# Optimization experiments

Measured on AMD Instinct MI355X. Metric: run time of the kernel, lower is better.

The kernel has to match this reference:

```python
import jax, jax.numpy as jnp
import numpy as np

INPUT_SIZE = 63
HIDDEN = 128
NUM_CLASSES = 11
B, T = 4096, 128


def _gru_layer(x_seq, w_ih, w_hh, b_ih, b_hh):
    """PyTorch-semantics GRU layer. x_seq: [B,T,D] -> outputs [B,T,H]."""
    Bsz = x_seq.shape[0]
    H = w_hh.shape[1]
    # Precompute input projections for all timesteps in one big GEMM: [B,T,3H]
    gates_x = jnp.einsum('btd,gd->btg', x_seq, w_ih) + b_ih

    def step(h, gx):
        gh = h @ w_hh.T + b_hh                       # [B,3H]
        xr, xz, xn = jnp.split(gx, 3, axis=-1)
        hr, hz, hn = jnp.split(gh, 3, axis=-1)
        r = jax.nn.sigmoid(xr + hr)
        z = jax.nn.sigmoid(xz + hz)
        n = jnp.tanh(xn + r * hn)
        h_new = (1.0 - z) * n + z * h
        return h_new, h_new

    h0 = jnp.zeros((Bsz, H), x_seq.dtype)
    _, ys = jax.lax.scan(step, h0, jnp.swapaxes(gates_x, 0, 1))  # ys: [T,B,H]
    return jnp.swapaxes(ys, 0, 1)


def setup_inputs() -> dict:
    key = jax.random.key(0)
    ks = jax.random.split(key, 13)
    s_ih0 = 1.0 / np.sqrt(HIDDEN)
    u = lambda k, shape, s: jax.random.uniform(k, shape, jnp.float32, -s, s)
    inp = {
        'x': jax.random.normal(ks[0], (B, T, INPUT_SIZE), jnp.float32),
        # GRU layer 0: input_size=63 -> hidden=128
        'w_ih0': u(ks[1], (3 * HIDDEN, INPUT_SIZE), s_ih0),
        'w_hh0': u(ks[2], (3 * HIDDEN, HIDDEN), s_ih0),
        'b_ih0': u(ks[3], (3 * HIDDEN,), s_ih0),
        'b_hh0': u(ks[4], (3 * HIDDEN,), s_ih0),
        # GRU layer 1: hidden -> hidden
        'w_ih1': u(ks[5], (3 * HIDDEN, HIDDEN), s_ih0),
        'w_hh1': u(ks[6], (3 * HIDDEN, HIDDEN), s_ih0),
        'b_ih1': u(ks[7], (3 * HIDDEN,), s_ih0),
        'b_hh1': u(ks[8], (3 * HIDDEN,), s_ih0),
        # classifier: Linear(128,64) -> ReLU -> Linear(64,11)
        'w1': u(ks[9], (64, HIDDEN), 1.0 / np.sqrt(HIDDEN)),
        'b1': u(ks[10], (64,), 1.0 / np.sqrt(HIDDEN)),
        'w2': u(ks[11], (NUM_CLASSES, 64), 1.0 / np.sqrt(64)),
        'b2': u(ks[12], (NUM_CLASSES,), 1.0 / np.sqrt(64)),
    }
    return inp


def reference(x, w_ih0, w_hh0, b_ih0, b_hh0, w_ih1, w_hh1, b_ih1, b_hh1, w1, b1, w2, b2):
    h1 = _gru_layer(x, w_ih0, w_hh0, b_ih0, b_hh0)    # [B,T,H]
    h2 = _gru_layer(h1, w_ih1, w_hh1, b_ih1, b_hh1)   # [B,T,H]
    last = h2[:, -1, :]                               # [B,H]
    hidden = jax.nn.relu(last @ w1.T + b1)            # [B,64] (dropout is identity in eval)
    return hidden @ w2.T + b2                         # [B,num_classes]
```

## Files before the change

### kernel.cpp

```cpp
#include <hip/hip_runtime.h>
#include <hip/hip_bf16.h>

typedef __attribute__((ext_vector_type(8))) short s8v;
typedef __attribute__((ext_vector_type(4))) float f4v;

#define MF(A, B, C) C = __builtin_amdgcn_mfma_f32_16x16x32_bf16((A), (B), (C), 0, 0, 0)

__device__ __forceinline__ ushort f2bf(float f) {
  unsigned u = __float_as_uint(f);
  u += 0x7FFF + ((u >> 16) & 1);
  return (ushort)(u >> 16);
}
__device__ __forceinline__ float bf2f(ushort h) {
  return __uint_as_float(((unsigned)h) << 16);
}
__device__ __forceinline__ float sigm(float p) { return 1.f / (1.f + __expf(-p)); }
__device__ __forceinline__ float tanh_safe(float a) {
  float t = __expf(-2.f * fabsf(a));
  float ng = (1.f - t) / (1.f + t);
  return a < 0.f ? -ng : ng;
}
__device__ __forceinline__ float dot4(float4 a, float4 b) {
  return fmaf(a.x, b.x, fmaf(a.y, b.y, fmaf(a.z, b.z, a.w * b.w)));
}

__global__ void conv_x(const float* __restrict__ x, ushort* __restrict__ xhi,
                       ushort* __restrict__ xlo, int total) {
  int idx = blockIdx.x * 256 + threadIdx.x;
  if (idx >= total) return;
  int k4 = (idx & 15) * 4;
  long bt = idx >> 4;
  #pragma unroll
  for (int j = 0; j < 4; ++j) {
    int k = k4 + j;
    float v = (k < 63) ? x[bt * 63 + k] : 0.f;
    ushort hi = f2bf(v);
    xhi[bt * 64 + k] = hi;
    xlo[bt * 64 + k] = f2bf(v - bf2f(hi));
  }
}

__global__ void pack_fr(const float* __restrict__ src, ushort* __restrict__ dst,
                        int Kreal, int KT, int total) {
  int idx = blockIdx.x * 256 + threadIdx.x;
  if (idx >= total) return;
  int i = idx & 7, l = (idx >> 3) & 63, hl = (idx >> 9) & 1;
  int rest = idx >> 10;
  int kt = rest % KT, nt = rest / KT;
  int g = nt * 16 + (l & 15);
  int k = kt * 32 + (l >> 4) * 8 + i;
  float v = (k < Kreal) ? src[g * Kreal + k] : 0.f;
  ushort hi = f2bf(v);
  dst[idx] = hl ? f2bf(v - bf2f(hi)) : hi;
}

__global__ void __attribute__((amdgpu_flat_work_group_size(512, 512),
                               amdgpu_waves_per_eu(2, 2)))
rec_l0(const ushort* __restrict__ xhi, const ushort* __restrict__ xlo,
       const ushort* __restrict__ fih, const ushort* __restrict__ fhh,
       const float* __restrict__ bi, const float* __restrict__ bh,
       ushort* __restrict__ s_hi, ushort* __restrict__ s_lo,
       ushort* __restrict__ c_hi, ushort* __restrict__ c_lo,
       int t0, int tc, int first)
{
  __shared__ __align__(16) ushort hh_[2][2048], hl_[2][2048];
  __shared__ __align__(16) float bb[512];
  const int tid = threadIdx.x;
  const int l = tid & 63, wv = tid >> 6;
  const int lr = l & 15, lg = l >> 4;
  const long b0 = (long)blockIdx.x * 16;

  if (tid < 128) {
    bb[tid]       = bi[tid] + bh[tid];
    bb[128 + tid] = bi[128 + tid] + bh[128 + tid];
    bb[256 + tid] = bi[256 + tid];
    bb[384 + tid] = bh[256 + tid];
  }
  const int u0 = (wv << 4) + (lg << 2);
  const int hb = lr * 256 + ((u0 << 1) ^ ((lr & 7) << 4));
  if (first) {
    *(ushort4*)((char*)hh_[0] + hb) = make_ushort4(0, 0, 0, 0);
    *(ushort4*)((char*)hl_[0] + hb) = make_ushort4(0, 0, 0, 0);
  } else {
    *(ushort4*)((char*)hh_[0] + hb) = *(const ushort4*)&c_hi[(b0 + lr) * 128 + u0];
    *(ushort4*)((char*)hl_[0] + hb) = *(const ushort4*)&c_lo[(b0 + lr) * 128 + u0];
  }

  s8v Ba[12];
  s8v Bb[24];
  #pragma unroll
  for (int gi = 0; gi < 3; ++gi) {
    int nt = wv + 8 * gi;
    #pragma unroll
    for (int kt = 0; kt < 2; ++kt)
      #pragma unroll
      for (int hl = 0; hl < 2; ++hl)
        Ba[(gi * 2 + kt) * 2 + hl] = *(const s8v*)&fih[((long)((nt * 2 + kt) * 2 + hl)) * 512 + l * 8];
    #pragma unroll
    for (int kt = 0; kt < 4; ++kt)
      #pragma unroll
      for (int hl = 0; hl < 2; ++hl)
        Bb[(gi * 4 + kt) * 2 + hl] = *(const s8v*)&fhh[((long)((nt * 4 + kt) * 2 + hl)) * 512 + l * 8];
  }

  s8v xch[2], xcl[2], xnh[2], xnl[2];
  {
    long xo = ((b0 + lr) * 128 + t0) * 64 + lg * 8;
    xch[0] = *(const s8v*)&xhi[xo]; xch[1] = *(const s8v*)&xhi[xo + 32];
    xcl[0] = *(const s8v*)&xlo[xo]; xcl[1] = *(const s8v*)&xlo[xo + 32];
  }
  __syncthreads();

  int pp = 0;
  for (int s = 0; s < tc; ++s, pp ^= 1) {
    if (s + 1 < tc) {
      long xo = ((b0 + lr) * 128 + (t0 + s + 1)) * 64 + lg * 8;
      xnh[0] = *(const s8v*)&xhi[xo]; xnh[1] = *(const s8v*)&xhi[xo + 32];
      xnl[0] = *(const s8v*)&xlo[xo]; xnl[1] = *(const s8v*)&xlo[xo + 32];
    }
    f4v ar = {0.f, 0.f, 0.f, 0.f}, az = ar, anx = ar, anh = ar;
    #pragma unroll
    for (int kt = 0; kt < 4; ++kt) {
      int ba = lr * 256 + ((kt * 64 + lg * 16) ^ ((lr & 7) << 4));
      s8v Ah = *(const s8v*)((const char*)hh_[pp] + ba);
      s8v Al = *(const s8v*)((const char*)hl_[pp] + ba);
      MF(Bb[(0 * 4 + kt) * 2 + 0], Ah, ar);
      MF(Bb[(1 * 4 + kt) * 2 + 0], Ah, az);
      MF(Bb[(2 * 4 + kt) * 2 + 0], Ah, anh);
      MF(Bb[(0 * 4 + kt) * 2 + 1], Ah, ar);
      MF(Bb[(1 * 4 + kt) * 2 + 1], Ah, az);
      MF(Bb[(2 * 4 + kt) * 2 + 1], Ah, anh);
      MF(Bb[(0 * 4 + kt) * 2 + 0], Al, ar);
      MF(Bb[(1 * 4 + kt) * 2 + 0], Al, az);
      MF(Bb[(2 * 4 + kt) * 2 + 0], Al, anh);
    }
    #pragma unroll
    for (int kt = 0; kt < 2; ++kt) {
      MF(Ba[(0 * 2 + kt) * 2 + 0], xch[kt], ar);
      MF(Ba[(1 * 2 + kt) * 2 + 0], xch[kt], az);
      MF(Ba[(2 * 2 + kt) * 2 + 0], xch[kt], anx);
      MF(Ba[(0 * 2 + kt) * 2 + 1], xch[kt], ar);
      MF(Ba[(1 * 2 + kt) * 2 + 1], xch[kt], az);
      MF(Ba[(2 * 2 + kt) * 2 + 1], xch[kt], anx);
      MF(Ba[(0 * 2 + kt) * 2 + 0], xcl[kt], ar);
      MF(Ba[(1 * 2 + kt) * 2 + 0], xcl[kt], az);
      MF(Ba[(2 * 2 + kt) * 2 + 0], xcl[kt], anx);
    }
    {
      ushort4 oh = *(const ushort4*)((const char*)hh_[pp] + hb);
      ushort4 ol = *(const ushort4*)((const char*)hl_[pp] + hb);
      f4v vbr = *(const f4v*)&bb[u0];
      f4v vbz = *(const f4v*)&bb[128 + u0];
      f4v vbx = *(const f4v*)&bb[256 + u0];
      f4v vbh = *(const f4v*)&bb[384 + u0];
      const ushort* ohp = (const ushort*)&oh;
      const ushort* olp = (const ushort*)&ol;
      ushort nh_[4], nl_[4];
      #pragma unroll
      for (int j = 0; j < 4; ++j) {
        float hold = bf2f(ohp[j]) + bf2f(olp[j]);
        float rg = sigm(ar[j] + vbr[j]);
        float zg = sigm(az[j] + vbz[j]);
        float ng = tanh_safe(anx[j] + vbx[j] + rg * (anh[j] + vbh[j]));
        float hn = (1.f - zg) * ng + zg * hold;
        ushort hbf = f2bf(hn);
        nh_[j] = hbf; nl_[j] = f2bf(hn - bf2f(hbf));
      }
      ushort4 wh = make_ushort4(nh_[0], nh_[1], nh_[2], nh_[3]);
      ushort4 wl = make_ushort4(nl_[0], nl_[1], nl_[2], nl_[3]);
      *(ushort4*)((char*)hh_[pp ^ 1] + hb) = wh;
      *(ushort4*)((char*)hl_[pp ^ 1] + hb) = wl;
      long so = ((long)s * 4096 + b0 + lr) * 128 + u0;
      *(ushort4*)&s_hi[so] = wh;
      *(ushort4*)&s_lo[so] = wl;
    }
    xch[0] = xnh[0]; xch[1] = xnh[1]; xcl[0] = xnl[0]; xcl[1] = xnl[1];
    __syncthreads();
  }
  *(ushort4*)&c_hi[(b0 + lr) * 128 + u0] = *(const ushort4*)((const char*)hh_[pp] + hb);
  *(ushort4*)&c_lo[(b0 + lr) * 128 + u0] = *(const ushort4*)((const char*)hl_[pp] + hb);
}

__global__ void __attribute__((amdgpu_flat_work_group_size(512, 512),
                               amdgpu_waves_per_eu(2, 2)))
rec_l1(const ushort* __restrict__ s_hi, const ushort* __restrict__ s_lo,
       const ushort* __restrict__ fih, const ushort* __restrict__ fhh,
       const float* __restrict__ bi, const float* __restrict__ bh,
       ushort* __restrict__ c_hi, ushort* __restrict__ c_lo,
       float* __restrict__ h1f, int tc, int first, int last)
{
  __shared__ __align__(16) ushort hh_[2][2048], hl_[2][2048];
  __shared__ __align__(16) ushort gh_[2][2048], gl_[2][2048];
  __shared__ __align__(16) float bb[512];
  const int tid = threadIdx.x;
  const int l = tid & 63, wv = tid >> 6;
  const int lr = l & 15, lg = l >> 4;
  const long b0 = (long)blockIdx.x * 16;

  if (tid < 128) {
    bb[tid]       = bi[tid] + bh[tid];
    bb[128 + tid] = bi[128 + tid] + bh[128 + tid];
    bb[256 + tid] = bi[256 + tid];
    bb[384 + tid] = bh[256 + tid];
  }
  const int u0 = (wv << 4) + (lg << 2);
  const int hb = lr * 256 + ((u0 << 1) ^ ((lr & 7) << 4));
  if (first) {
    *(ushort4*)((char*)hh_[0] + hb) = make_ushort4(0, 0, 0, 0);
    *(ushort4*)((char*)hl_[0] + hb) = make_ushort4(0, 0, 0, 0);
  } else {
    *(ushort4*)((char*)hh_[0] + hb) = *(const ushort4*)&c_hi[(b0 + lr) * 128 + u0];
    *(ushort4*)((char*)hl_[0] + hb) = *(const ushort4*)&c_lo[(b0 + lr) * 128 + u0];
  }

  const int stid = tid & 255;
  const int srow = stid >> 4, sc16 = stid & 15;
  const int sdst = srow * 256 + ((sc16 * 16) ^ ((srow & 7) << 4));
  const ushort* ssel = (tid < 256) ? s_hi : s_lo;
  ushort* dsel = (tid < 256) ? &gh_[0][0] : &gl_[0][0];

  s8v Ba[24], Bb[24];
  #pragma unroll
  for (int gi = 0; gi < 3; ++gi) {
    int nt = wv + 8 * gi;
    #pragma unroll
    for (int kt = 0; kt < 4; ++kt)
      #pragma unroll
      for (int hl = 0; hl < 2; ++hl) {
        Ba[(gi * 4 + kt) * 2 + hl] = *(const s8v*)&fih[((long)((nt * 4 + kt) * 2 + hl)) * 512 + l * 8];
        Bb[(gi * 4 + kt) * 2 + hl] = *(const s8v*)&fhh[((long)((nt * 4 + kt) * 2 + hl)) * 512 + l * 8];
      }
  }
  {
    s8v v = *(const s8v*)&ssel[((long)0 * 4096 + b0 + srow) * 128 + sc16 * 8];
    *(s8v*)((char*)(dsel + 0 * 2048) + sdst) = v;
  }
  __syncthreads();

  int pp = 0;
  for (int tl = 0; tl < tc; ++tl, pp ^= 1) {
    s8v sreg;
    const int havenext = (tl + 1 < tc);
    if (havenext)
      sreg = *(const s8v*)&ssel[((long)(tl + 1) * 4096 + b0 + srow) * 128 + sc16 * 8];

    f4v ar = {0.f, 0.f, 0.f, 0.f}, az = ar, anx = ar, anh = ar;
    #pragma unroll
    for (int kt = 0; kt < 4; ++kt) {
      int ba = lr * 256 + ((kt * 64 + lg * 16) ^ ((lr & 7) << 4));
      s8v Hh = *(const s8v*)((const char*)hh_[pp] + ba);
      s8v Hl = *(const s8v*)((const char*)hl_[pp] + ba);
      s8v Gh = *(const s8v*)((const char*)gh_[pp] + ba);
      s8v Gl = *(const s8v*)((const char*)gl_[pp] + ba);
      MF(Bb[(0 * 4 + kt) * 2 + 0], Hh, ar);
      MF(Ba[(0 * 4 + kt) * 2 + 0], Gh, ar);
      MF(Bb[(1 * 4 + kt) * 2 + 0], Hh, az);
      MF(Ba[(1 * 4 + kt) * 2 + 0], Gh, az);
      MF(Bb[(2 * 4 + kt) * 2 + 0], Hh, anh);
      MF(Ba[(2 * 4 + kt) * 2 + 0], Gh, anx);
      MF(Bb[(0 * 4 + kt) * 2 + 1], Hh, ar);
      MF(Ba[(0 * 4 + kt) * 2 + 1], Gh, ar);
      MF(Bb[(1 * 4 + kt) * 2 + 1], Hh, az);
      MF(Ba[(1 * 4 + kt) * 2 + 1], Gh, az);
      MF(Bb[(2 * 4 + kt) * 2 + 1], Hh, anh);
      MF(Ba[(2 * 4 + kt) * 2 + 1], Gh, anx);
      MF(Bb[(0 * 4 + kt) * 2 + 0], Hl, ar);
      MF(Ba[(0 * 4 + kt) * 2 + 0], Gl, ar);
      MF(Bb[(1 * 4 + kt) * 2 + 0], Hl, az);
      MF(Ba[(1 * 4 + kt) * 2 + 0], Gl, az);
      MF(Bb[(2 * 4 + kt) * 2 + 0], Hl, anh);
      MF(Ba[(2 * 4 + kt) * 2 + 0], Gl, anx);
    }
    {
      ushort4 oh = *(const ushort4*)((const char*)hh_[pp] + hb);
      ushort4 ol = *(const ushort4*)((const char*)hl_[pp] + hb);
      f4v vbr = *(const f4v*)&bb[u0];
      f4v vbz = *(const f4v*)&bb[128 + u0];
      f4v vbx = *(const f4v*)&bb[256 + u0];
      f4v vbh = *(const f4v*)&bb[384 + u0];
      const ushort* ohp = (const ushort*)&oh;
      const ushort* olp = (const ushort*)&ol;
      ushort nh_[4], nl_[4];
      #pragma unroll
      for (int j = 0; j < 4; ++j) {
        float hold = bf2f(ohp[j]) + bf2f(olp[j]);
        float rg = sigm(ar[j] + vbr[j]);
        float zg = sigm(az[j] + vbz[j]);
        float ng = tanh_safe(anx[j] + vbx[j] + rg * (anh[j] + vbh[j]));
        float hn = (1.f - zg) * ng + zg * hold;
        ushort hbf = f2bf(hn);
        nh_[j] = hbf; nl_[j] = f2bf(hn - bf2f(hbf));
      }
      *(ushort4*)((char*)hh_[pp ^ 1] + hb) = make_ushort4(nh_[0], nh_[1], nh_[2], nh_[3]);
      *(ushort4*)((char*)hl_[pp ^ 1] + hb) = make_ushort4(nl_[0], nl_[1], nl_[2], nl_[3]);
    }
    if (havenext)
      *(s8v*)((char*)(dsel + (size_t)(pp ^ 1) * 2048) + sdst) = sreg;
    __syncthreads();
  }
  {
    ushort4 fh = *(const ushort4*)((const char*)hh_[pp] + hb);
    ushort4 fl = *(const ushort4*)((const char*)hl_[pp] + hb);
    *(ushort4*)&c_hi[(b0 + lr) * 128 + u0] = fh;
    *(ushort4*)&c_lo[(b0 + lr) * 128 + u0] = fl;
    if (last) {
      const ushort* fhp = (const ushort*)&fh;
      const ushort* flp = (const ushort*)&fl;
      float4 o;
      o.x = bf2f(fhp[0]) + bf2f(flp[0]);
      o.y = bf2f(fhp[1]) + bf2f(flp[1]);
      o.z = bf2f(fhp[2]) + bf2f(flp[2]);
      o.w = bf2f(fhp[3]) + bf2f(flp[3]);
      *(float4*)&h1f[(b0 + lr) * 128 + u0] = o;
    }
  }
}

__global__ __launch_bounds__(512) void head_k(
    const float* __restrict__ h1f, const float* __restrict__ w1,
    const float* __restrict__ b1, const float* __restrict__ w2,
    const float* __restrict__ b2, float* __restrict__ out)
{
  __shared__ float hrow[16][132];
  __shared__ float w1s[64][132];
  __shared__ float hid[16][68];
  const int tid = threadIdx.x;
  const long b0 = (long)blockIdx.x * 16;
  for (int i = tid; i < 64 * 128; i += 512) w1s[i >> 7][i & 127] = w1[i];
  {
    int rr = tid >> 5, k4 = (tid & 31) * 4;
    *(float4*)&hrow[rr][k4] = *(const float4*)&h1f[(b0 + rr) * 128 + k4];
  }
  __syncthreads();
  {
    int r = tid & 15, fu = tid >> 4;
    float a0 = 0.f, a1 = 0.f;
    for (int k4 = 0; k4 < 32; ++k4) {
      float4 hv = *(const float4*)&hrow[r][k4 * 4];
      float4 wa = *(const float4*)&w1s[fu][k4 * 4];
      float4 wb = *(const float4*)&w1s[fu + 32][k4 * 4];
      a0 += dot4(wa, hv);
      a1 += dot4(wb, hv);
    }
    a0 += b1[fu]; a1 += b1[fu + 32];
    hid[r][fu]      = fmaxf(a0, 0.f);
    hid[r][fu + 32] = fmaxf(a1, 0.f);
  }
  __syncthreads();
  if (tid < 176) {
    int rr = tid / 11, c = tid - rr * 11;
    float acc = b2[c];
    for (int k = 0; k < 64; ++k) acc = fmaf(w2[c * 64 + k], hid[rr][k], acc);
    out[(b0 + rr) * 11 + c] = acc;
  }
}

extern "C" void kernel_launch(void* const* d_in, const int* in_sizes, int n_in,
                              void* d_out, int out_size, void* d_ws, size_t ws_size,
                              hipStream_t stream) {
  (void)in_sizes; (void)n_in; (void)out_size;
  const float* x    = (const float*)d_in[0];
  const float* wih0 = (const float*)d_in[1];
  const float* whh0 = (const float*)d_in[2];
  const float* bih0 = (const float*)d_in[3];
  const float* bhh0 = (const float*)d_in[4];
  const float* wih1 = (const float*)d_in[5];
  const float* whh1 = (const float*)d_in[6];
  const float* bih1 = (const float*)d_in[7];
  const float* bhh1 = (const float*)d_in[8];
  const float* w1   = (const float*)d_in[9];
  const float* b1   = (const float*)d_in[10];
  const float* w2   = (const float*)d_in[11];
  const float* b2   = (const float*)d_in[12];

  char* wsb = (char*)d_ws;
  size_t o = 0;
  ushort* fih0 = (ushort*)(wsb + o); o += 98304;
  ushort* fhh0 = (ushort*)(wsb + o); o += 196608;
  ushort* fih1 = (ushort*)(wsb + o); o += 196608;
  ushort* fhh1 = (ushort*)(wsb + o); o += 196608;
  ushort* xhi  = (ushort*)(wsb + o); o += 67108864ULL;
  ushort* xlo  = (ushort*)(wsb + o); o += 67108864ULL;
  ushort* hc0h = (ushort*)(wsb + o); o += 1048576;
  ushort* hc0l = (ushort*)(wsb + o); o += 1048576;
  ushort* hc1h = (ushort*)(wsb + o); o += 1048576;
  ushort* hc1l = (ushort*)(wsb + o); o += 1048576;
  float*  h1f  = (float*)(wsb + o);  o += 2097152;

  long rem = (long)ws_size - (long)o;
  long tcmax = rem / (2 * 1048576L);
  int Tc = tcmax > 128 ? 128 : (int)tcmax;
  if (Tc < 1) return;
  ushort* sh = (ushort*)(wsb + o);
  ushort* sl = sh + (long)Tc * 524288;

  hipLaunchKernelGGL(conv_x, dim3(32768), dim3(256), 0, stream, x, xhi, xlo, 8388608);
  hipLaunchKernelGGL(pack_fr, dim3(192), dim3(256), 0, stream, wih0, fih0, 63, 2, 49152);
  hipLaunchKernelGGL(pack_fr, dim3(384), dim3(256), 0, stream, whh0, fhh0, 128, 4, 98304);
  hipLaunchKernelGGL(pack_fr, dim3(384), dim3(256), 0, stream, wih1, fih1, 128, 4, 98304);
  hipLaunchKernelGGL(pack_fr, dim3(384), dim3(256), 0, stream, whh1, fhh1, 128, 4, 98304);

  for (int t0 = 0; t0 < 128; t0 += Tc) {
    int tc = (128 - t0) < Tc ? (128 - t0) : Tc;
    hipLaunchKernelGGL(rec_l0, dim3(256), dim3(512), 0, stream,
                       xhi, xlo, fih0, fhh0, bih0, bhh0, sh, sl, hc0h, hc0l,
                       t0, tc, (int)(t0 == 0));
    hipLaunchKernelGGL(rec_l1, dim3(256), dim3(512), 0, stream,
                       sh, sl, fih1, fhh1, bih1, bhh1, hc1h, hc1l, h1f,
                       tc, (int)(t0 == 0), (int)(t0 + tc == 128));
  }
  hipLaunchKernelGGL(head_k, dim3(256), dim3(512), 0, stream,
                     h1f, w1, b1, w2, b2, (float*)d_out);
}
```

Before: 676.0 us.

## Split layer-0 GRU recurrence MFMAs across two wave groups with LDS reduction

Doubles the rec_l0 block to 1024 threads. Eight waves compute the hi-weight products and the hi·lo cross term, while eight more compute the lo-weight products and write partial sums to shared memory. The hi waves then add those partials and apply the gate math. The extra waves also stage the next timestep of x into shared memory, replacing per-lane global loads. This halves weight registers and MFMA chain length per wave, which should shorten the serial per-step latency. The cost is an extra block barrier per step plus an LDS round trip for the partials.

```diff
diff --git a/kernel.cpp b/kernel.cpp
--- a/kernel.cpp
+++ b/kernel.cpp
@@ -54,8 +54,8 @@
   dst[idx] = hl ? f2bf(v - bf2f(hi)) : hi;
 }
 
-__global__ void __attribute__((amdgpu_flat_work_group_size(512, 512),
-                               amdgpu_waves_per_eu(2, 2)))
+__global__ void __attribute__((amdgpu_flat_work_group_size(1024, 1024),
+                               amdgpu_waves_per_eu(4, 4)))
 rec_l0(const ushort* __restrict__ xhi, const ushort* __restrict__ xlo,
        const ushort* __restrict__ fih, const ushort* __restrict__ fhh,
        const float* __restrict__ bi, const float* __restrict__ bh,
@@ -65,9 +65,15 @@
 {
   __shared__ __align__(16) ushort hh_[2][2048], hl_[2][2048];
   __shared__ __align__(16) float bb[512];
+  __shared__ __align__(16) ushort xs[2][2][16][76];
+  __shared__ __align__(16) float pd[8][4][256];
+
   const int tid = threadIdx.x;
-  const int l = tid & 63, wv = tid >> 6;
+  const int wv = tid >> 6, l = tid & 63;
   const int lr = l & 15, lg = l >> 4;
+  const int isHi = (wv < 8);
+  const int p = wv & 7;
+  const int lsw = l ^ (l >> 3);
   const long b0 = (long)blockIdx.x * 16;
 
   if (tid < 128) {
@@ -76,77 +82,103 @@
     bb[256 + tid] = bi[256 + tid];
     bb[384 + tid] = bh[256 + tid];
   }
-  const int u0 = (wv << 4) + (lg << 2);
+  const int u0 = (p << 4) + (lg << 2);
   const int hb = lr * 256 + ((u0 << 1) ^ ((lr & 7) << 4));
-  if (first) {
-    *(ushort4*)((char*)hh_[0] + hb) = make_ushort4(0, 0, 0, 0);
-    *(ushort4*)((char*)hl_[0] + hb) = make_ushort4(0, 0, 0, 0);
-  } else {
-    *(ushort4*)((char*)hh_[0] + hb) = *(const ushort4*)&c_hi[(b0 + lr) * 128 + u0];
-    *(ushort4*)((char*)hl_[0] + hb) = *(const ushort4*)&c_lo[(b0 + lr) * 128 + u0];
-  }
-
-  s8v Ba[12];
-  s8v Bb[24];
+  if (isHi) {
+    if (first) {
+      *(ushort4*)((char*)hh_[0] + hb) = make_ushort4(0, 0, 0, 0);
+      *(ushort4*)((char*)hl_[0] + hb) = make_ushort4(0, 0, 0, 0);
+    } else {
+      *(ushort4*)((char*)hh_[0] + hb) = *(const ushort4*)&c_hi[(b0 + lr) * 128 + u0];
+      *(ushort4*)((char*)hl_[0] + hb) = *(const ushort4*)&c_lo[(b0 + lr) * 128 + u0];
+    }
+  }
+
+  const int hls = isHi ? 0 : 1;
+  s8v Fih[6];
+  s8v Fhh[12];
   #pragma unroll
   for (int gi = 0; gi < 3; ++gi) {
-    int nt = wv + 8 * gi;
+    int nt = p + 8 * gi;
     #pragma unroll
     for (int kt = 0; kt < 2; ++kt)
-      #pragma unroll
-      for (int hl = 0; hl < 2; ++hl)
-        Ba[(gi * 2 + kt) * 2 + hl] = *(const s8v*)&fih[((long)((nt * 2 + kt) * 2 + hl)) * 512 + l * 8];
+      Fih[gi * 2 + kt] = *(const s8v*)&fih[((long)((nt * 2 + kt) * 2 + hls)) * 512 + l * 8];
     #pragma unroll
     for (int kt = 0; kt < 4; ++kt)
-      #pragma unroll
-      for (int hl = 0; hl < 2; ++hl)
-        Bb[(gi * 4 + kt) * 2 + hl] = *(const s8v*)&fhh[((long)((nt * 4 + kt) * 2 + hl)) * 512 + l * 8];
-  }
-
-  s8v xch[2], xcl[2], xnh[2], xnl[2];
-  {
-    long xo = ((b0 + lr) * 128 + t0) * 64 + lg * 8;
-    xch[0] = *(const s8v*)&xhi[xo]; xch[1] = *(const s8v*)&xhi[xo + 32];
-    xcl[0] = *(const s8v*)&xlo[xo]; xcl[1] = *(const s8v*)&xlo[xo + 32];
+      Fhh[gi * 4 + kt] = *(const s8v*)&fhh[((long)((nt * 4 + kt) * 2 + hls)) * 512 + l * 8];
+  }
+
+  const int sid = (wv - 8) * 64 + l;
+  const int spl = sid >> 8, sq = sid & 255;
+  const int srow = sq >> 4, sc8 = sq & 15;
+  const ushort* xsrc = spl ? xlo : xhi;
+
+  if (!isHi) {
+    ushort4 v = *(const ushort4*)&xsrc[((b0 + srow) * 128 + t0) * 64 + sc8 * 4];
+    *(ushort4*)&xs[0][spl][srow][sc8 * 4] = v;
   }
   __syncthreads();
 
   int pp = 0;
   for (int s = 0; s < tc; ++s, pp ^= 1) {
-    if (s + 1 < tc) {
-      long xo = ((b0 + lr) * 128 + (t0 + s + 1)) * 64 + lg * 8;
-      xnh[0] = *(const s8v*)&xhi[xo]; xnh[1] = *(const s8v*)&xhi[xo + 32];
-      xnl[0] = *(const s8v*)&xlo[xo]; xnl[1] = *(const s8v*)&xlo[xo + 32];
-    }
+    const int havenext = (s + 1 < tc);
+    ushort4 xr;
+    if (!isHi && havenext)
+      xr = *(const ushort4*)&xsrc[((b0 + srow) * 128 + (t0 + s + 1)) * 64 + sc8 * 4];
+
     f4v ar = {0.f, 0.f, 0.f, 0.f}, az = ar, anx = ar, anh = ar;
-    #pragma unroll
-    for (int kt = 0; kt < 4; ++kt) {
-      int ba = lr * 256 + ((kt * 64 + lg * 16) ^ ((lr & 7) << 4));
-      s8v Ah = *(const s8v*)((const char*)hh_[pp] + ba);
-      s8v Al = *(const s8v*)((const char*)hl_[pp] + ba);
-      MF(Bb[(0 * 4 + kt) * 2 + 0], Ah, ar);
-      MF(Bb[(1 * 4 + kt) * 2 + 0], Ah, az);
-      MF(Bb[(2 * 4 + kt) * 2 + 0], Ah, anh);
-      MF(Bb[(0 * 4 + kt) * 2 + 1], Ah, ar);
-      MF(Bb[(1 * 4 + kt) * 2 + 1], Ah, az);
-      MF(Bb[(2 * 4 + kt) * 2 + 1], Ah, anh);
-      MF(Bb[(0 * 4 + kt) * 2 + 0], Al, ar);
-      MF(Bb[(1 * 4 + kt) * 2 + 0], Al, az);
-      MF(Bb[(2 * 4 + kt) * 2 + 0], Al, anh);
-    }
-    #pragma unroll
-    for (int kt = 0; kt < 2; ++kt) {
-      MF(Ba[(0 * 2 + kt) * 2 + 0], xch[kt], ar);
-      MF(Ba[(1 * 2 + kt) * 2 + 0], xch[kt], az);
-      MF(Ba[(2 * 2 + kt) * 2 + 0], xch[kt], anx);
-      MF(Ba[(0 * 2 + kt) * 2 + 1], xch[kt], ar);
-      MF(Ba[(1 * 2 + kt) * 2 + 1], xch[kt], az);
-      MF(Ba[(2 * 2 + kt) * 2 + 1], xch[kt], anx);
-      MF(Ba[(0 * 2 + kt) * 2 + 0], xcl[kt], ar);
-      MF(Ba[(1 * 2 + kt) * 2 + 0], xcl[kt], az);
-      MF(Ba[(2 * 2 + kt) * 2 + 0], xcl[kt], anx);
-    }
-    {
+    if (isHi) {
+      #pragma unroll
+      for (int kt = 0; kt < 4; ++kt) {
+        int ba = lr * 256 + ((kt * 64 + lg * 16) ^ ((lr & 7) << 4));
+        s8v Ah = *(const s8v*)((const char*)hh_[pp] + ba);
+        s8v Al = *(const s8v*)((const char*)hl_[pp] + ba);
+        MF(Fhh[0 * 4 + kt], Ah, ar);
+        MF(Fhh[1 * 4 + kt], Ah, az);
+        MF(Fhh[2 * 4 + kt], Ah, anh);
+        MF(Fhh[0 * 4 + kt], Al, ar);
+        MF(Fhh[1 * 4 + kt], Al, az);
+        MF(Fhh[2 * 4 + kt], Al, anh);
+      }
+      #pragma unroll
+      for (int kt = 0; kt < 2; ++kt) {
+        s8v xh = *(const s8v*)&xs[pp][0][lr][kt * 32 + lg * 8];
+        s8v xl = *(const s8v*)&xs[pp][1][lr][kt * 32 + lg * 8];
+        MF(Fih[0 * 2 + kt], xh, ar);
+        MF(Fih[1 * 2 + kt], xh, az);
+        MF(Fih[2 * 2 + kt], xh, anx);
+        MF(Fih[0 * 2 + kt], xl, ar);
+        MF(Fih[1 * 2 + kt], xl, az);
+        MF(Fih[2 * 2 + kt], xl, anx);
+      }
+    } else {
+      #pragma unroll
+      for (int kt = 0; kt < 4; ++kt) {
+        int ba = lr * 256 + ((kt * 64 + lg * 16) ^ ((lr & 7) << 4));
+        s8v Ah = *(const s8v*)((const char*)hh_[pp] + ba);
+        MF(Fhh[0 * 4 + kt], Ah, ar);
+        MF(Fhh[1 * 4 + kt], Ah, az);
+        MF(Fhh[2 * 4 + kt], Ah, anh);
+      }
+      #pragma unroll
+      for (int kt = 0; kt < 2; ++kt) {
+        s8v xh = *(const s8v*)&xs[pp][0][lr][kt * 32 + lg * 8];
+        MF(Fih[0 * 2 + kt], xh, ar);
+        MF(Fih[1 * 2 + kt], xh, az);
+        MF(Fih[2 * 2 + kt], xh, anx);
+      }
+      ((f4v*)pd[p][0])[lsw] = ar;
+      ((f4v*)pd[p][1])[lsw] = az;
+      ((f4v*)pd[p][2])[lsw] = anx;
+      ((f4v*)pd[p][3])[lsw] = anh;
+    }
+    __syncthreads();
+
+    if (isHi) {
+      ar  += ((const f4v*)pd[p][0])[lsw];
+      az  += ((const f4v*)pd[p][1])[lsw];
+      anx += ((const f4v*)pd[p][2])[lsw];
+      anh += ((const f4v*)pd[p][3])[lsw];
       ushort4 oh = *(const ushort4*)((const char*)hh_[pp] + hb);
       ushort4 ol = *(const ushort4*)((const char*)hl_[pp] + hb);
       f4v vbr = *(const f4v*)&bb[u0];
@@ -173,12 +205,15 @@
       long so = ((long)s * 4096 + b0 + lr) * 128 + u0;
       *(ushort4*)&s_hi[so] = wh;
       *(ushort4*)&s_lo[so] = wl;
-    }
-    xch[0] = xnh[0]; xch[1] = xnh[1]; xcl[0] = xnl[0]; xcl[1] = xnl[1];
+    } else if (havenext) {
+      *(ushort4*)&xs[pp ^ 1][spl][srow][sc8 * 4] = xr;
+    }
     __syncthreads();
   }
-  *(ushort4*)&c_hi[(b0 + lr) * 128 + u0] = *(const ushort4*)((const char*)hh_[pp] + hb);
-  *(ushort4*)&c_lo[(b0 + lr) * 128 + u0] = *(const ushort4*)((const char*)hl_[pp] + hb);
+  if (isHi) {
+    *(ushort4*)&c_hi[(b0 + lr) * 128 + u0] = *(const ushort4*)((const char*)hh_[pp] + hb);
+    *(ushort4*)&c_lo[(b0 + lr) * 128 + u0] = *(const ushort4*)((const char*)hl_[pp] + hb);
+  }
 }
 
 __global__ void __attribute__((amdgpu_flat_work_group_size(512, 512),
@@ -402,7 +437,7 @@
 
   for (int t0 = 0; t0 < 128; t0 += Tc) {
     int tc = (128 - t0) < Tc ? (128 - t0) : Tc;
-    hipLaunchKernelGGL(rec_l0, dim3(256), dim3(512), 0, stream,
+    hipLaunchKernelGGL(rec_l0, dim3(256), dim3(1024), 0, stream,
                        xhi, xlo, fih0, fhh0, bih0, bhh0, sh, sl, hc0h, hc0l,
                        t0, tc, (int)(t0 == 0));
     hipLaunchKernelGGL(rec_l1, dim3(256), dim3(512), 0, stream,
```

Result: slower. 1.008 ms (+49.1%).

## Load layer-1 input directly from global into MFMA registers, defer layer-0 stores

Applied to the files above, without the earlier changes.

Layer 1 no longer stages the layer-0 output sequence through double-buffered shared memory. Each wave loads its MFMA A-operand fragments straight from global memory each step, split into two halves so the second half overlaps the hidden-state MFMAs. In layer 0, the per-step global stores of the hidden state are moved to the start of the next iteration so they are issued away from the barrier. This removes LDS traffic and shared-memory footprint, but puts global-load latency directly on the recurrent critical path and has every wave fetch the same input redundantly.

```diff
diff --git a/kernel.cpp b/kernel.cpp
--- a/kernel.cpp
+++ b/kernel.cpp
@@ -111,8 +111,15 @@
   }
   __syncthreads();
 
+  const long sbase = (b0 + lr) * 128 + u0;
+  ushort4 st_h, st_l;
+
   int pp = 0;
   for (int s = 0; s < tc; ++s, pp ^= 1) {
+    if (s > 0) {
+      *(ushort4*)&s_hi[sbase + (long)(s - 1) * 524288] = st_h;
+      *(ushort4*)&s_lo[sbase + (long)(s - 1) * 524288] = st_l;
+    }
     if (s + 1 < tc) {
       long xo = ((b0 + lr) * 128 + (t0 + s + 1)) * 64 + lg * 8;
       xnh[0] = *(const s8v*)&xhi[xo]; xnh[1] = *(const s8v*)&xhi[xo + 32];
@@ -170,13 +177,13 @@
       ushort4 wl = make_ushort4(nl_[0], nl_[1], nl_[2], nl_[3]);
       *(ushort4*)((char*)hh_[pp ^ 1] + hb) = wh;
       *(ushort4*)((char*)hl_[pp ^ 1] + hb) = wl;
-      long so = ((long)s * 4096 + b0 + lr) * 128 + u0;
-      *(ushort4*)&s_hi[so] = wh;
-      *(ushort4*)&s_lo[so] = wl;
+      st_h = wh; st_l = wl;
     }
     xch[0] = xnh[0]; xch[1] = xnh[1]; xcl[0] = xnl[0]; xcl[1] = xnl[1];
     __syncthreads();
   }
+  *(ushort4*)&s_hi[sbase + (long)(tc - 1) * 524288] = st_h;
+  *(ushort4*)&s_lo[sbase + (long)(tc - 1) * 524288] = st_l;
   *(ushort4*)&c_hi[(b0 + lr) * 128 + u0] = *(const ushort4*)((const char*)hh_[pp] + hb);
   *(ushort4*)&c_lo[(b0 + lr) * 128 + u0] = *(const ushort4*)((const char*)hl_[pp] + hb);
 }
@@ -190,7 +197,6 @@
        float* __restrict__ h1f, int tc, int first, int last)
 {
   __shared__ __align__(16) ushort hh_[2][2048], hl_[2][2048];
-  __shared__ __align__(16) ushort gh_[2][2048], gl_[2][2048];
   __shared__ __align__(16) float bb[512];
   const int tid = threadIdx.x;
   const int l = tid & 63, wv = tid >> 6;
@@ -213,12 +219,6 @@
     *(ushort4*)((char*)hl_[0] + hb) = *(const ushort4*)&c_lo[(b0 + lr) * 128 + u0];
   }
 
-  const int stid = tid & 255;
-  const int srow = stid >> 4, sc16 = stid & 15;
-  const int sdst = srow * 256 + ((sc16 * 16) ^ ((srow & 7) << 4));
-  const ushort* ssel = (tid < 256) ? s_hi : s_lo;
-  ushort* dsel = (tid < 256) ? &gh_[0][0] : &gl_[0][0];
-
   s8v Ba[24], Bb[24];
   #pragma unroll
   for (int gi = 0; gi < 3; ++gi) {
@@ -231,18 +231,16 @@
         Bb[(gi * 4 + kt) * 2 + hl] = *(const s8v*)&fhh[((long)((nt * 4 + kt) * 2 + hl)) * 512 + l * 8];
       }
   }
-  {
-    s8v v = *(const s8v*)&ssel[((long)0 * 4096 + b0 + srow) * 128 + sc16 * 8];
-    *(s8v*)((char*)(dsel + 0 * 2048) + sdst) = v;
-  }
   __syncthreads();
+
+  const long gbase0 = (b0 + lr) * 128 + lg * 8;
 
   int pp = 0;
   for (int tl = 0; tl < tc; ++tl, pp ^= 1) {
-    s8v sreg;
-    const int havenext = (tl + 1 < tc);
-    if (havenext)
-      sreg = *(const s8v*)&ssel[((long)(tl + 1) * 4096 + b0 + srow) * 128 + sc16 * 8];
+    const long gb = (long)tl * 524288 + gbase0;
+    s8v Gh[4], Gl[4];
+    Gh[0] = *(const s8v*)&s_hi[gb];        Gh[1] = *(const s8v*)&s_hi[gb + 32];
+    Gl[0] = *(const s8v*)&s_lo[gb];        Gl[1] = *(const s8v*)&s_lo[gb + 32];
 
     f4v ar = {0.f, 0.f, 0.f, 0.f}, az = ar, anx = ar, anh = ar;
     #pragma unroll
@@ -250,26 +248,31 @@
       int ba = lr * 256 + ((kt * 64 + lg * 16) ^ ((lr & 7) << 4));
       s8v Hh = *(const s8v*)((const char*)hh_[pp] + ba);
       s8v Hl = *(const s8v*)((const char*)hl_[pp] + ba);
-      s8v Gh = *(const s8v*)((const char*)gh_[pp] + ba);
-      s8v Gl = *(const s8v*)((const char*)gl_[pp] + ba);
       MF(Bb[(0 * 4 + kt) * 2 + 0], Hh, ar);
-      MF(Ba[(0 * 4 + kt) * 2 + 0], Gh, ar);
       MF(Bb[(1 * 4 + kt) * 2 + 0], Hh, az);
-      MF(Ba[(1 * 4 + kt) * 2 + 0], Gh, az);
       MF(Bb[(2 * 4 + kt) * 2 + 0], Hh, anh);
-      MF(Ba[(2 * 4 + kt) * 2 + 0], Gh, anx);
       MF(Bb[(0 * 4 + kt) * 2 + 1], Hh, ar);
-      MF(Ba[(0 * 4 + kt) * 2 + 1], Gh, ar);
       MF(Bb[(1 * 4 + kt) * 2 + 1], Hh, az);
-      MF(Ba[(1 * 4 + kt) * 2 + 1], Gh, az);
       MF(Bb[(2 * 4 + kt) * 2 + 1], Hh, anh);
-      MF(Ba[(2 * 4 + kt) * 2 + 1], Gh, anx);
       MF(Bb[(0 * 4 + kt) * 2 + 0], Hl, ar);
-      MF(Ba[(0 * 4 + kt) * 2 + 0], Gl, ar);
       MF(Bb[(1 * 4 + kt) * 2 + 0], Hl, az);
-      MF(Ba[(1 * 4 + kt) * 2 + 0], Gl, az);
       MF(Bb[(2 * 4 + kt) * 2 + 0], Hl, anh);
-      MF(Ba[(2 * 4 + kt) * 2 + 0], Gl, anx);
+      if (kt == 1) {
+        Gh[2] = *(const s8v*)&s_hi[gb + 64];  Gh[3] = *(const s8v*)&s_hi[gb + 96];
+        Gl[2] = *(const s8v*)&s_lo[gb + 64];  Gl[3] = *(const s8v*)&s_lo[gb + 96];
+      }
+    }
+    #pragma unroll
+    for (int kt = 0; kt < 4; ++kt) {
+      MF(Ba[(0 * 4 + kt) * 2 + 0], Gh[kt], ar);
+      MF(Ba[(1 * 4 + kt) * 2 + 0], Gh[kt], az);
+      MF(Ba[(2 * 4 + kt) * 2 + 0], Gh[kt], anx);
+      MF(Ba[(0 * 4 + kt) * 2 + 1], Gh[kt], ar);
+      MF(Ba[(1 * 4 + kt) * 2 + 1], Gh[kt], az);
+      MF(Ba[(2 * 4 + kt) * 2 + 1], Gh[kt], anx);
+      MF(Ba[(0 * 4 + kt) * 2 + 0], Gl[kt], ar);
+      MF(Ba[(1 * 4 + kt) * 2 + 0], Gl[kt], az);
+      MF(Ba[(2 * 4 + kt) * 2 + 0], Gl[kt], anx);
     }
     {
       ushort4 oh = *(const ushort4*)((const char*)hh_[pp] + hb);
@@ -294,8 +297,6 @@
       *(ushort4*)((char*)hh_[pp ^ 1] + hb) = make_ushort4(nh_[0], nh_[1], nh_[2], nh_[3]);
       *(ushort4*)((char*)hl_[pp ^ 1] + hb) = make_ushort4(nl_[0], nl_[1], nl_[2], nl_[3]);
     }
-    if (havenext)
-      *(s8v*)((char*)(dsel + (size_t)(pp ^ 1) * 2048) + sdst) = sreg;
     __syncthreads();
   }
   {
```

After: 922.4 us. 1.36x slower.

## Fuse input bf16 hi/lo split into layer-0 recurrence and defer sequence stores

Applied to the files above, without the earlier changes.

Drops the separate conv_x pass that wrote hi/lo bf16 copies of x to workspace. rec_l0 now prefetches the fp32 input rows for the next step and splits them into hi/lo bf16 fragments in registers after the gate math. Each step's sequence-output stores are delayed by one iteration so they overlap with the next step's work. This removes a large write and re-read of converted input through memory, at the cost of unaligned float4 loads (the row stride is 63 floats), extra ALU work per step and more register pressure.

```diff
diff --git a/kernel.cpp b/kernel.cpp
--- a/kernel.cpp
+++ b/kernel.cpp
@@ -22,22 +22,6 @@
 }
 __device__ __forceinline__ float dot4(float4 a, float4 b) {
   return fmaf(a.x, b.x, fmaf(a.y, b.y, fmaf(a.z, b.z, a.w * b.w)));
-}
-
-__global__ void conv_x(const float* __restrict__ x, ushort* __restrict__ xhi,
-                       ushort* __restrict__ xlo, int total) {
-  int idx = blockIdx.x * 256 + threadIdx.x;
-  if (idx >= total) return;
-  int k4 = (idx & 15) * 4;
-  long bt = idx >> 4;
-  #pragma unroll
-  for (int j = 0; j < 4; ++j) {
-    int k = k4 + j;
-    float v = (k < 63) ? x[bt * 63 + k] : 0.f;
-    ushort hi = f2bf(v);
-    xhi[bt * 64 + k] = hi;
-    xlo[bt * 64 + k] = f2bf(v - bf2f(hi));
-  }
 }
 
 __global__ void pack_fr(const float* __restrict__ src, ushort* __restrict__ dst,
@@ -56,7 +40,7 @@
 
 __global__ void __attribute__((amdgpu_flat_work_group_size(512, 512),
                                amdgpu_waves_per_eu(2, 2)))
-rec_l0(const ushort* __restrict__ xhi, const ushort* __restrict__ xlo,
+rec_l0(const float* __restrict__ x,
        const ushort* __restrict__ fih, const ushort* __restrict__ fhh,
        const float* __restrict__ bi, const float* __restrict__ bh,
        ushort* __restrict__ s_hi, ushort* __restrict__ s_lo,
@@ -103,21 +87,46 @@
         Bb[(gi * 4 + kt) * 2 + hl] = *(const s8v*)&fhh[((long)((nt * 4 + kt) * 2 + hl)) * 512 + l * 8];
   }
 
-  s8v xch[2], xcl[2], xnh[2], xnl[2];
-  {
-    long xo = ((b0 + lr) * 128 + t0) * 64 + lg * 8;
-    xch[0] = *(const s8v*)&xhi[xo]; xch[1] = *(const s8v*)&xhi[xo + 32];
-    xcl[0] = *(const s8v*)&xlo[xo]; xcl[1] = *(const s8v*)&xlo[xo + 32];
-  }
+  float4 nf0, nf1, nf2, nf3;
+  auto loadx = [&](int t) {
+    long xr = ((b0 + lr) * 128 + t) * 63;
+    nf0 = *(const float4*)&x[xr + lg * 8];
+    nf1 = *(const float4*)&x[xr + lg * 8 + 4];
+    if (lg < 3) {
+      nf2 = *(const float4*)&x[xr + 32 + lg * 8];
+      nf3 = *(const float4*)&x[xr + 32 + lg * 8 + 4];
+    } else {
+      nf2 = *(const float4*)&x[xr + 56];
+      float4 t4 = *(const float4*)&x[xr + 59];
+      nf3 = make_float4(t4.y, t4.z, t4.w, 0.f);
+    }
+  };
+  auto cvt8 = [](const float4& a, const float4& b, s8v& hi, s8v& lo) {
+    float v0[8] = {a.x, a.y, a.z, a.w, b.x, b.y, b.z, b.w};
+    #pragma unroll
+    for (int i = 0; i < 8; ++i) {
+      ushort h = f2bf(v0[i]);
+      hi[i] = (short)h;
+      lo[i] = (short)f2bf(v0[i] - bf2f(h));
+    }
+  };
+
+  s8v xch[2], xcl[2];
+  loadx(t0);
+  cvt8(nf0, nf1, xch[0], xcl[0]);
+  cvt8(nf2, nf3, xch[1], xcl[1]);
   __syncthreads();
+
+  const long sbase = (b0 + lr) * 128 + u0;
+  ushort4 st_h, st_l;
 
   int pp = 0;
   for (int s = 0; s < tc; ++s, pp ^= 1) {
-    if (s + 1 < tc) {
-      long xo = ((b0 + lr) * 128 + (t0 + s + 1)) * 64 + lg * 8;
-      xnh[0] = *(const s8v*)&xhi[xo]; xnh[1] = *(const s8v*)&xhi[xo + 32];
-      xnl[0] = *(const s8v*)&xlo[xo]; xnl[1] = *(const s8v*)&xlo[xo + 32];
-    }
+    if (s > 0) {
+      *(ushort4*)&s_hi[sbase + (long)(s - 1) * 524288] = st_h;
+      *(ushort4*)&s_lo[sbase + (long)(s - 1) * 524288] = st_l;
+    }
+    if (s + 1 < tc) loadx(t0 + s + 1);
     f4v ar = {0.f, 0.f, 0.f, 0.f}, az = ar, anx = ar, anh = ar;
     #pragma unroll
     for (int kt = 0; kt < 4; ++kt) {
@@ -170,13 +179,16 @@
       ushort4 wl = make_ushort4(nl_[0], nl_[1], nl_[2], nl_[3]);
       *(ushort4*)((char*)hh_[pp ^ 1] + hb) = wh;
       *(ushort4*)((char*)hl_[pp ^ 1] + hb) = wl;
-      long so = ((long)s * 4096 + b0 + lr) * 128 + u0;
-      *(ushort4*)&s_hi[so] = wh;
-      *(ushort4*)&s_lo[so] = wl;
-    }
-    xch[0] = xnh[0]; xch[1] = xnh[1]; xcl[0] = xnl[0]; xcl[1] = xnl[1];
+      st_h = wh; st_l = wl;
+    }
+    if (s + 1 < tc) {
+      cvt8(nf0, nf1, xch[0], xcl[0]);
+      cvt8(nf2, nf3, xch[1], xcl[1]);
+    }
     __syncthreads();
   }
+  *(ushort4*)&s_hi[sbase + (long)(tc - 1) * 524288] = st_h;
+  *(ushort4*)&s_lo[sbase + (long)(tc - 1) * 524288] = st_l;
   *(ushort4*)&c_hi[(b0 + lr) * 128 + u0] = *(const ushort4*)((const char*)hh_[pp] + hb);
   *(ushort4*)&c_lo[(b0 + lr) * 128 + u0] = *(const ushort4*)((const char*)hl_[pp] + hb);
 }
@@ -379,8 +391,6 @@
   ushort* fhh0 = (ushort*)(wsb + o); o += 196608;
   ushort* fih1 = (ushort*)(wsb + o); o += 196608;
   ushort* fhh1 = (ushort*)(wsb + o); o += 196608;
-  ushort* xhi  = (ushort*)(wsb + o); o += 67108864ULL;
-  ushort* xlo  = (ushort*)(wsb + o); o += 67108864ULL;
   ushort* hc0h = (ushort*)(wsb + o); o += 1048576;
   ushort* hc0l = (ushort*)(wsb + o); o += 1048576;
   ushort* hc1h = (ushort*)(wsb + o); o += 1048576;
@@ -394,7 +404,6 @@
   ushort* sh = (ushort*)(wsb + o);
   ushort* sl = sh + (long)Tc * 524288;
 
-  hipLaunchKernelGGL(conv_x, dim3(32768), dim3(256), 0, stream, x, xhi, xlo, 8388608);
   hipLaunchKernelGGL(pack_fr, dim3(192), dim3(256), 0, stream, wih0, fih0, 63, 2, 49152);
   hipLaunchKernelGGL(pack_fr, dim3(384), dim3(256), 0, stream, whh0, fhh0, 128, 4, 98304);
   hipLaunchKernelGGL(pack_fr, dim3(384), dim3(256), 0, stream, wih1, fih1, 128, 4, 98304);
@@ -403,7 +412,7 @@
   for (int t0 = 0; t0 < 128; t0 += Tc) {
     int tc = (128 - t0) < Tc ? (128 - t0) : Tc;
     hipLaunchKernelGGL(rec_l0, dim3(256), dim3(512), 0, stream,
-                       xhi, xlo, fih0, fhh0, bih0, bhh0, sh, sl, hc0h, hc0l,
+                       x, fih0, fhh0, bih0, bhh0, sh, sl, hc0h, hc0l,
                        t0, tc, (int)(t0 == 0));
     hipLaunchKernelGGL(rec_l1, dim3(256), dim3(512), 0, stream,
                        sh, sl, fih1, fhh1, bih1, bhh1, hc1h, hc1l, h1f,
```

After: 750.7 us. 11.1% more time.
